# Kernel tuning notes

Measured on AMD Instinct MI355X. Metric: run time of the kernel, lower is better.

## Reference

```python
import jax, jax.numpy as jnp
import numpy as np

S, B, D = 2048, 256, 128


def setup_inputs() -> dict:
    key = jax.random.key(0)
    ks = jax.random.split(key, 5)
    scale = 1.0 / np.sqrt(D)
    return {
        "src": jax.random.normal(ks[0], (S, B, D), dtype=jnp.float32),
        "Wm": jax.random.normal(ks[1], (D, D), dtype=jnp.float32) * scale,
        "bm": jax.random.normal(ks[2], (D,), dtype=jnp.float32) * scale,
        "Wb": jax.random.normal(ks[3], (2 * D, D), dtype=jnp.float32) * (1.0 / np.sqrt(2 * D)),
        "bb": jax.random.normal(ks[4], (D,), dtype=jnp.float32) * scale,
    }


def reference(src, Wm, bm, Wb, bb):
    # h = relu(map(src)) : [S, B, D]
    h = jax.nn.relu(jnp.einsum('sbd,de->sbe', src, Wm) + bm)
    # bracket of all adjacent pairs: relu(Linear(cat(h[i], h[i+1])))
    pairs = jnp.concatenate([h[:-1], h[1:]], axis=-1)          # [S-1, B, 2D]
    tmp = jax.nn.relu(jnp.einsum('sbf,fe->sbe', pairs, Wb) + bb)  # [S-1, B, D]
    # running context: context_i = sum_{j<=i} (h[j] + tmp[j])
    return jnp.cumsum(h[:-1] + tmp, axis=0)                    # [S-1, B, D]
```

## Files before the change

### kernel.cpp

```cpp
#include <hip/hip_runtime.h>


#define S_DIM 2048
#define B_DIM 256
#define D_DIM 128
#define SM1   2047
#define NCOL  (B_DIM * D_DIM)
#define NSEG  64
#define SEGLEN 32

typedef __attribute__((ext_vector_type(8))) short bf16x8;
typedef __attribute__((ext_vector_type(4))) float f32x4;

__device__ inline short f2bf(float x) {
    unsigned u = __builtin_bit_cast(unsigned, x);
    unsigned r = (u + 0x7fffu + ((u >> 16) & 1u)) >> 16;
    return (short)r;
}
__device__ inline float bf2f(short v) {
    unsigned u = ((unsigned)(unsigned short)v) << 16;
    return __builtin_bit_cast(float, u);
}

__global__ __launch_bounds__(256) void k0_prep(const float* __restrict__ Wm,
                                               const float* __restrict__ Wb,
                                               short* __restrict__ Wm_sw,
                                               short* __restrict__ Wb_sw) {
    int idx = blockIdx.x * 256 + threadIdx.x;
    if (idx < 16384) {
        int j = idx & 7, lane = (idx >> 3) & 63, kt = (idx >> 9) & 3, nt = idx >> 11;
        int k = kt * 32 + ((lane >> 4) << 3) + j;
        int n = nt * 16 + (lane & 15);
        Wm_sw[idx] = f2bf(Wm[k * D_DIM + n]);
    }
    if (idx < 32768) {
        int half = idx >> 14;
        int r = idx & 16383;
        int j = r & 7, lane = (r >> 3) & 63, kt = (r >> 9) & 3, nt = r >> 11;
        int k = kt * 32 + ((lane >> 4) << 3) + j;
        int n = nt * 16 + (lane & 15);
        Wb_sw[idx] = f2bf(Wb[(half * 128 + k) * D_DIM + n]);
    }
}

#define K1_RT 8
__global__ __launch_bounds__(256, 4) void k1_h(const float* __restrict__ src,
                                               const short* __restrict__ Wm_sw,
                                               const float* __restrict__ bm,
                                               short* __restrict__ h) {
    const int lane = threadIdx.x & 63;
    const int wave = threadIdx.x >> 6;
    const int m = lane & 15;
    const int quad = lane >> 4;
    const int wbase = wave * 32;
    const int n0 = wave * 2;

    bf16x8 bw[2][4];
#pragma unroll
    for (int n = 0; n < 2; ++n)
#pragma unroll
        for (int kt = 0; kt < 4; ++kt)
            bw[n][kt] = *(const bf16x8*)(Wm_sw + ((size_t)((n0 + n) * 4 + kt) * 64 + lane) * 8);

    const float bias0 = bm[wbase + m];
    const float bias1 = bm[wbase + 16 + m];

#pragma unroll 1
    for (int r = 0; r < K1_RT; ++r) {
        const int rowBase = blockIdx.x * (16 * K1_RT) + r * 16;
        const float* arow = src + (size_t)(rowBase + m) * D_DIM + quad * 8;

        bf16x8 a[4];
#pragma unroll
        for (int kt = 0; kt < 4; ++kt) {
            float4 lo = *(const float4*)(arow + kt * 32);
            float4 hi = *(const float4*)(arow + kt * 32 + 4);
            a[kt][0] = f2bf(lo.x); a[kt][1] = f2bf(lo.y);
            a[kt][2] = f2bf(lo.z); a[kt][3] = f2bf(lo.w);
            a[kt][4] = f2bf(hi.x); a[kt][5] = f2bf(hi.y);
            a[kt][6] = f2bf(hi.z); a[kt][7] = f2bf(hi.w);
        }

        f32x4 acc0 = (f32x4){0.f, 0.f, 0.f, 0.f};
        f32x4 acc1 = (f32x4){0.f, 0.f, 0.f, 0.f};
#pragma unroll
        for (int kt = 0; kt < 4; ++kt) {
            acc0 = __builtin_amdgcn_mfma_f32_16x16x32_bf16(a[kt], bw[0][kt], acc0, 0, 0, 0);
            acc1 = __builtin_amdgcn_mfma_f32_16x16x32_bf16(a[kt], bw[1][kt], acc1, 0, 0, 0);
        }

        short* hout = h + (size_t)(rowBase + quad * 4) * D_DIM;
#pragma unroll
        for (int i = 0; i < 4; ++i) {
            float v0 = acc0[i] + bias0;
            v0 = v0 > 0.f ? v0 : 0.f;
            hout[(size_t)i * D_DIM + wbase + m] = f2bf(v0);
            float v1 = acc1[i] + bias1;
            v1 = v1 > 0.f ? v1 : 0.f;
            hout[(size_t)i * D_DIM + wbase + 16 + m] = f2bf(v1);
        }
    }
}

__global__ __launch_bounds__(256, 4) void k2_fused(const short* __restrict__ h,
                                                   const short* __restrict__ Wb_sw,
                                                   const float* __restrict__ bb,
                                                   float* __restrict__ g,
                                                   float* __restrict__ segsum) {
    const int lane = threadIdx.x & 63;
    const int wave = threadIdx.x >> 6;
    const int m = lane & 15;
    const int quad = lane >> 4;
    const int seg = blockIdx.x >> 4;
    const int rB = (blockIdx.x & 15) * 16;
    const int wbase = wave * 32;
    const int n0 = wave * 2;

    bf16x8 bw0[2][4];
#pragma unroll
    for (int n = 0; n < 2; ++n)
#pragma unroll
        for (int kt = 0; kt < 4; ++kt)
            bw0[n][kt] = *(const bf16x8*)(Wb_sw + ((size_t)((n0 + n) * 4 + kt) * 64 + lane) * 8);
    const short* wb1 = Wb_sw + 16384;

    const float bias0 = bb[wbase + m];
    const float bias1 = bb[wbase + 16 + m];

    f32x4 sa0 = (f32x4){0.f, 0.f, 0.f, 0.f};
    f32x4 sa1 = (f32x4){0.f, 0.f, 0.f, 0.f};

    const int s0 = seg * SEGLEN;
    const int send = min(s0 + SEGLEN, SM1);

#pragma unroll 1
    for (int s = s0; s < send; ++s) {
        const short* h0 = h + ((size_t)s * B_DIM + rB + m) * D_DIM + quad * 8;

        bf16x8 a[4];
#pragma unroll
        for (int kt = 0; kt < 4; ++kt) a[kt] = *(const bf16x8*)(h0 + kt * 32);

        f32x4 acc0 = (f32x4){0.f, 0.f, 0.f, 0.f};
        f32x4 acc1 = (f32x4){0.f, 0.f, 0.f, 0.f};
#pragma unroll
        for (int kt = 0; kt < 4; ++kt) {
            acc0 = __builtin_amdgcn_mfma_f32_16x16x32_bf16(a[kt], bw0[0][kt], acc0, 0, 0, 0);
            acc1 = __builtin_amdgcn_mfma_f32_16x16x32_bf16(a[kt], bw0[1][kt], acc1, 0, 0, 0);
        }

        const short* h1 = h0 + (size_t)B_DIM * D_DIM;
#pragma unroll
        for (int kt = 0; kt < 4; ++kt) a[kt] = *(const bf16x8*)(h1 + kt * 32);
#pragma unroll
        for (int kt = 0; kt < 4; ++kt) {
            bf16x8 b0 = *(const bf16x8*)(wb1 + ((size_t)(n0 * 4 + kt) * 64 + lane) * 8);
            acc0 = __builtin_amdgcn_mfma_f32_16x16x32_bf16(a[kt], b0, acc0, 0, 0, 0);
            bf16x8 b1 = *(const bf16x8*)(wb1 + ((size_t)((n0 + 1) * 4 + kt) * 64 + lane) * 8);
            acc1 = __builtin_amdgcn_mfma_f32_16x16x32_bf16(a[kt], b1, acc1, 0, 0, 0);
        }

        const short* hr = h + ((size_t)s * B_DIM + rB + quad * 4) * D_DIM;
        float* gr = g + ((size_t)s * NCOL + (size_t)(rB + quad * 4) * D_DIM);
#pragma unroll
        for (int i = 0; i < 4; ++i) {
            float v0 = acc0[i] + bias0;
            v0 = v0 > 0.f ? v0 : 0.f;
            v0 += bf2f(hr[(size_t)i * D_DIM + wbase + m]);
            gr[(size_t)i * D_DIM + wbase + m] = v0;
            sa0[i] += v0;

            float v1 = acc1[i] + bias1;
            v1 = v1 > 0.f ? v1 : 0.f;
            v1 += bf2f(hr[(size_t)i * D_DIM + wbase + 16 + m]);
            gr[(size_t)i * D_DIM + wbase + 16 + m] = v1;
            sa1[i] += v1;
        }
    }

    float* ss = segsum + (size_t)seg * NCOL + (size_t)(rB + quad * 4) * D_DIM;
#pragma unroll
    for (int i = 0; i < 4; ++i) {
        ss[(size_t)i * D_DIM + wbase + m] = sa0[i];
        ss[(size_t)i * D_DIM + wbase + 16 + m] = sa1[i];
    }
}

__global__ __launch_bounds__(256) void k3_prefix(float* __restrict__ segsum) {
    int col = blockIdx.x * 256 + threadIdx.x;
    float acc = 0.f;
#pragma unroll 4
    for (int j = 0; j < NSEG; ++j) {
        size_t idx = (size_t)j * NCOL + col;
        float v = segsum[idx];
        segsum[idx] = acc;
        acc += v;
    }
}

__global__ __launch_bounds__(256) void k4_apply(float* __restrict__ g,
                                                const float* __restrict__ segsum) {
    int t = blockIdx.x * 256 + threadIdx.x;
    int c4 = (t & 8191) * 4;
    int seg = t >> 13;
    int s0 = seg * SEGLEN;
    int send = min(s0 + SEGLEN, SM1);

    f32x4 acc = *(const f32x4*)(segsum + (size_t)seg * NCOL + c4);
#pragma unroll 1
    for (int s = s0; s < send; ++s) {
        float* p = g + (size_t)s * NCOL + c4;
        f32x4 v = *(const f32x4*)p;
        acc += v;
        *(f32x4*)p = acc;
    }
}

extern "C" void kernel_launch(void* const* d_in, const int* in_sizes, int n_in,
                              void* d_out, int out_size, void* d_ws, size_t ws_size,
                              hipStream_t stream) {
    const float* src = (const float*)d_in[0];
    const float* Wm  = (const float*)d_in[1];
    const float* bm  = (const float*)d_in[2];
    const float* Wb  = (const float*)d_in[3];
    const float* bb  = (const float*)d_in[4];
    float* out = (float*)d_out;

    char* ws = (char*)d_ws;
    short* h       = (short*)(ws);
    float* segsum  = (float*)(ws + 134217728ull);
    short* Wm_sw   = (short*)(ws + 142606336ull);
    short* Wb_sw   = (short*)(ws + 142639104ull);

    hipLaunchKernelGGL(k0_prep, dim3(128), dim3(256), 0, stream, Wm, Wb, Wm_sw, Wb_sw);
    hipLaunchKernelGGL(k1_h, dim3((S_DIM * B_DIM) / (16 * K1_RT)), dim3(256), 0, stream,
                       src, Wm_sw, bm, h);
    hipLaunchKernelGGL(k2_fused, dim3(NSEG * 16), dim3(256), 0, stream,
                       h, Wb_sw, bb, out, segsum);
    hipLaunchKernelGGL(k3_prefix, dim3(NCOL / 256), dim3(256), 0, stream, segsum);
    hipLaunchKernelGGL(k4_apply, dim3((NSEG * (NCOL / 4)) / 256), dim3(256), 0, stream,
                       out, segsum);
}
```

Measured before the change: 801.7 us.

## Recompute bracket GEMM in second pass instead of storing and rereading partials

The scan changes from write-partials-then-apply to reduce-then-rescan. The first pass computes only per-segment sums without writing the output. After the segment prefix, a second pass recomputes the GEMM and writes the final cumulative values directly. This removes one full read-modify-write of the large fp32 output in exchange for running the bracket GEMM twice. Blocks now use 8 waves with one 16-column slice each, the second Wb half is kept in registers, next-row h loads are prefetched, and the prefix kernel loads all segments before writing.

Result: no change. 786.0 us (-2.0%).

```diff
diff --git a/kernel.cpp b/kernel.cpp
--- a/kernel.cpp
+++ b/kernel.cpp
@@ -102,117 +102,104 @@
     }
 }
 
-__global__ __launch_bounds__(256, 4) void k2_fused(const short* __restrict__ h,
-                                                   const short* __restrict__ Wb_sw,
-                                                   const float* __restrict__ bb,
-                                                   float* __restrict__ g,
-                                                   float* __restrict__ segsum) {
+template<bool WRITE_OUT>
+__global__ __launch_bounds__(512, 4) void k2_core(const short* __restrict__ h,
+                                                  const short* __restrict__ Wb_sw,
+                                                  const float* __restrict__ bb,
+                                                  const float* __restrict__ segpre,
+                                                  float* __restrict__ segsum,
+                                                  float* __restrict__ out) {
     const int lane = threadIdx.x & 63;
-    const int wave = threadIdx.x >> 6;
+    const int n = threadIdx.x >> 6;
     const int m = lane & 15;
     const int quad = lane >> 4;
     const int seg = blockIdx.x >> 4;
     const int rB = (blockIdx.x & 15) * 16;
-    const int wbase = wave * 32;
-    const int n0 = wave * 2;
-
-    bf16x8 bw0[2][4];
-#pragma unroll
-    for (int n = 0; n < 2; ++n)
-#pragma unroll
-        for (int kt = 0; kt < 4; ++kt)
-            bw0[n][kt] = *(const bf16x8*)(Wb_sw + ((size_t)((n0 + n) * 4 + kt) * 64 + lane) * 8);
-    const short* wb1 = Wb_sw + 16384;
-
-    const float bias0 = bb[wbase + m];
-    const float bias1 = bb[wbase + 16 + m];
-
-    f32x4 sa0 = (f32x4){0.f, 0.f, 0.f, 0.f};
-    f32x4 sa1 = (f32x4){0.f, 0.f, 0.f, 0.f};
+
+    bf16x8 bw0[4], bw1[4];
+#pragma unroll
+    for (int kt = 0; kt < 4; ++kt) {
+        bw0[kt] = *(const bf16x8*)(Wb_sw + ((size_t)(n * 4 + kt) * 64 + lane) * 8);
+        bw1[kt] = *(const bf16x8*)(Wb_sw + 16384 + ((size_t)(n * 4 + kt) * 64 + lane) * 8);
+    }
+    const float bias = bb[n * 16 + m];
 
     const int s0 = seg * SEGLEN;
     const int send = min(s0 + SEGLEN, SM1);
 
+    f32x4 sacc;
+    if (WRITE_OUT) {
+        const float* sp = segpre + (size_t)seg * NCOL + (size_t)(rB + quad * 4) * D_DIM + n * 16 + m;
+#pragma unroll
+        for (int i = 0; i < 4; ++i) sacc[i] = sp[(size_t)i * D_DIM];
+    } else {
+        sacc = (f32x4){0.f, 0.f, 0.f, 0.f};
+    }
+
+    bf16x8 A0[4], A1[4];
+    {
+        const short* p0 = h + ((size_t)s0 * B_DIM + rB + m) * D_DIM + quad * 8;
+        const short* p1 = p0 + (size_t)B_DIM * D_DIM;
+#pragma unroll
+        for (int kt = 0; kt < 4; ++kt) { A0[kt] = *(const bf16x8*)(p0 + kt * 32); A1[kt] = *(const bf16x8*)(p1 + kt * 32); }
+    }
+
+#define K2_STEP(CUR, NXT, SS, PF)                                                              \
+    {                                                                                          \
+        const int s_ = (SS);                                                                   \
+        f32x4 acc = (f32x4){0.f, 0.f, 0.f, 0.f};                                               \
+        _Pragma("unroll")                                                                      \
+        for (int kt = 0; kt < 4; ++kt)                                                         \
+            acc = __builtin_amdgcn_mfma_f32_16x16x32_bf16(CUR[kt], bw0[kt], acc, 0, 0, 0);     \
+        if (PF) {                                \
+            const int sp_ = min(s_ + 2, SM1);                                                  \
+            const short* pp = h + ((size_t)sp_ * B_DIM + rB + m) * D_DIM + quad * 8;           \
+            _Pragma("unroll")                                                                  \
+            for (int kt = 0; kt < 4; ++kt) CUR[kt] = *(const bf16x8*)(pp + kt * 32);           \
+        }                                                                                      \
+        _Pragma("unroll")                                                                      \
+        for (int kt = 0; kt < 4; ++kt)                                                         \
+            acc = __builtin_amdgcn_mfma_f32_16x16x32_bf16(NXT[kt], bw1[kt], acc, 0, 0, 0);     \
+        const short* hr = h + ((size_t)s_ * B_DIM + rB + quad * 4) * D_DIM + n * 16 + m;       \
+        float* orow = out + ((size_t)s_ * NCOL + (size_t)(rB + quad * 4) * D_DIM + n * 16 + m);\
+        _Pragma("unroll")                                                                      \
+        for (int i = 0; i < 4; ++i) {                                                          \
+            float v = acc[i] + bias;                                                           \
+            v = v > 0.f ? v : 0.f;                                                             \
+            v += bf2f(hr[(size_t)i * D_DIM]);                                                  \
+            sacc[i] += v;                                                                      \
+            if (WRITE_OUT) orow[(size_t)i * D_DIM] = sacc[i];                                  \
+        }                                                                                      \
+    }
+
+    int s = s0;
 #pragma unroll 1
-    for (int s = s0; s < send; ++s) {
-        const short* h0 = h + ((size_t)s * B_DIM + rB + m) * D_DIM + quad * 8;
-
-        bf16x8 a[4];
-#pragma unroll
-        for (int kt = 0; kt < 4; ++kt) a[kt] = *(const bf16x8*)(h0 + kt * 32);
-
-        f32x4 acc0 = (f32x4){0.f, 0.f, 0.f, 0.f};
-        f32x4 acc1 = (f32x4){0.f, 0.f, 0.f, 0.f};
-#pragma unroll
-        for (int kt = 0; kt < 4; ++kt) {
-            acc0 = __builtin_amdgcn_mfma_f32_16x16x32_bf16(a[kt], bw0[0][kt], acc0, 0, 0, 0);
-            acc1 = __builtin_amdgcn_mfma_f32_16x16x32_bf16(a[kt], bw0[1][kt], acc1, 0, 0, 0);
-        }
-
-        const short* h1 = h0 + (size_t)B_DIM * D_DIM;
-#pragma unroll
-        for (int kt = 0; kt < 4; ++kt) a[kt] = *(const bf16x8*)(h1 + kt * 32);
-#pragma unroll
-        for (int kt = 0; kt < 4; ++kt) {
-            bf16x8 b0 = *(const bf16x8*)(wb1 + ((size_t)(n0 * 4 + kt) * 64 + lane) * 8);
-            acc0 = __builtin_amdgcn_mfma_f32_16x16x32_bf16(a[kt], b0, acc0, 0, 0, 0);
-            bf16x8 b1 = *(const bf16x8*)(wb1 + ((size_t)((n0 + 1) * 4 + kt) * 64 + lane) * 8);
-            acc1 = __builtin_amdgcn_mfma_f32_16x16x32_bf16(a[kt], b1, acc1, 0, 0, 0);
-        }
-
-        const short* hr = h + ((size_t)s * B_DIM + rB + quad * 4) * D_DIM;
-        float* gr = g + ((size_t)s * NCOL + (size_t)(rB + quad * 4) * D_DIM);
-#pragma unroll
-        for (int i = 0; i < 4; ++i) {
-            float v0 = acc0[i] + bias0;
-            v0 = v0 > 0.f ? v0 : 0.f;
-            v0 += bf2f(hr[(size_t)i * D_DIM + wbase + m]);
-            gr[(size_t)i * D_DIM + wbase + m] = v0;
-            sa0[i] += v0;
-
-            float v1 = acc1[i] + bias1;
-            v1 = v1 > 0.f ? v1 : 0.f;
-            v1 += bf2f(hr[(size_t)i * D_DIM + wbase + 16 + m]);
-            gr[(size_t)i * D_DIM + wbase + 16 + m] = v1;
-            sa1[i] += v1;
-        }
-    }
-
-    float* ss = segsum + (size_t)seg * NCOL + (size_t)(rB + quad * 4) * D_DIM;
-#pragma unroll
-    for (int i = 0; i < 4; ++i) {
-        ss[(size_t)i * D_DIM + wbase + m] = sa0[i];
-        ss[(size_t)i * D_DIM + wbase + 16 + m] = sa1[i];
+    for (; s + 2 <= send; s += 2) {
+        K2_STEP(A0, A1, s, 1)
+        K2_STEP(A1, A0, s + 1, 1)
+    }
+    if (s < send) {
+        K2_STEP(A0, A1, s, 0)
+    }
+#undef K2_STEP
+
+    if (!WRITE_OUT) {
+        float* ss = segsum + (size_t)seg * NCOL + (size_t)(rB + quad * 4) * D_DIM + n * 16 + m;
+#pragma unroll
+        for (int i = 0; i < 4; ++i) ss[(size_t)i * D_DIM] = sacc[i];
     }
 }
 
 __global__ __launch_bounds__(256) void k3_prefix(float* __restrict__ segsum) {
     int col = blockIdx.x * 256 + threadIdx.x;
+    float v[NSEG];
+#pragma unroll
+    for (int j = 0; j < NSEG; ++j) v[j] = segsum[(size_t)j * NCOL + col];
     float acc = 0.f;
-#pragma unroll 4
+#pragma unroll
     for (int j = 0; j < NSEG; ++j) {
-        size_t idx = (size_t)j * NCOL + col;
-        float v = segsum[idx];
-        segsum[idx] = acc;
-        acc += v;
-    }
-}
-
-__global__ __launch_bounds__(256) void k4_apply(float* __restrict__ g,
-                                                const float* __restrict__ segsum) {
-    int t = blockIdx.x * 256 + threadIdx.x;
-    int c4 = (t & 8191) * 4;
-    int seg = t >> 13;
-    int s0 = seg * SEGLEN;
-    int send = min(s0 + SEGLEN, SM1);
-
-    f32x4 acc = *(const f32x4*)(segsum + (size_t)seg * NCOL + c4);
-#pragma unroll 1
-    for (int s = s0; s < send; ++s) {
-        float* p = g + (size_t)s * NCOL + c4;
-        f32x4 v = *(const f32x4*)p;
-        acc += v;
-        *(f32x4*)p = acc;
+        segsum[(size_t)j * NCOL + col] = acc;
+        acc += v[j];
     }
 }
 
@@ -235,9 +222,9 @@
     hipLaunchKernelGGL(k0_prep, dim3(128), dim3(256), 0, stream, Wm, Wb, Wm_sw, Wb_sw);
     hipLaunchKernelGGL(k1_h, dim3((S_DIM * B_DIM) / (16 * K1_RT)), dim3(256), 0, stream,
                        src, Wm_sw, bm, h);
-    hipLaunchKernelGGL(k2_fused, dim3(NSEG * 16), dim3(256), 0, stream,
-                       h, Wb_sw, bb, out, segsum);
+    hipLaunchKernelGGL((k2_core<false>), dim3(NSEG * 16), dim3(512), 0, stream,
+                       h, Wb_sw, bb, (const float*)nullptr, segsum, out);
     hipLaunchKernelGGL(k3_prefix, dim3(NCOL / 256), dim3(256), 0, stream, segsum);
-    hipLaunchKernelGGL(k4_apply, dim3((NSEG * (NCOL / 4)) / 256), dim3(256), 0, stream,
-                       out, segsum);
-}
+    hipLaunchKernelGGL((k2_core<true>), dim3(NSEG * 16), dim3(512), 0, stream,
+                       h, Wb_sw, bb, (const float*)segsum, (float*)nullptr, out);
+}
```
